# Performance work log

Measured on AMD Instinct MI355X. Metric: run time of the kernel, lower is better.

## Reference

```python
import jax, jax.numpy as jnp
import numpy as np

N_NODES = 100000
N_EDGES = 3200000
D_FEAT = 128


def setup_inputs() -> dict:
    key = jax.random.key(0)
    k1, k2, k3 = jax.random.split(key, 3)
    edges = jax.random.randint(k1, (2, N_EDGES), 0, N_NODES, dtype=jnp.int64)
    attentions = jax.random.uniform(k2, (N_EDGES,), dtype=jnp.float32)
    X = jax.random.normal(k3, (N_NODES, D_FEAT), dtype=jnp.float32)
    return {"edges": edges, "attentions": attentions, "N": N_NODES, "X": X}


def reference(edges, attentions, N, X):
    # Sparse COO adjacency (rows=edges[0], cols=edges[1], vals=attentions)
    # times dense X: out[i] = sum over edges (i -> j) of att_e * X[j]
    src = edges[0]  # row index i
    dst = edges[1]  # col index j
    messages = attentions[:, None] * X[dst]          # [E, D] gather + weight
    out = jax.ops.segment_sum(messages, src, num_segments=N)  # [N, D] scatter-add
    return out
```

## Files before the change

kernel.cpp:

```cpp
#include <hip/hip_runtime.h>

typedef unsigned int u32;
typedef unsigned short u16;


constexpr int D_FEAT  = 128;
constexpr int N_NODES = 100000;
constexpr int BROWS   = 128;
constexpr int KB      = (N_NODES + BROWS - 1) / BROWS;
constexpr int CHUNK   = 8192;
constexpr int NGRP    = 8;
constexpr int NCONV   = 128;
constexpr int CAP     = 4608;
constexpr int RPT     = CAP / 512;
constexpr int NPAN    = 8;
constexpr int NCELL   = NPAN * BROWS;

__device__ __forceinline__ u32 rne_bf16(float f) {
    u32 u = __float_as_uint(f);
    return (u + 0x7FFFu + ((u >> 16) & 1u)) >> 16;
}

__device__ __forceinline__ u32 pack_rec(int s, int d, float a) {
    u32 q = (u32)(a * 255.0f + 0.5f);
    return ((u32)(s & 127) << 25) | ((u32)d << 8) | q;
}

__device__ __forceinline__ u32 cell_of(u32 rec) {
    return (((rec >> 22) & 7u) << 7) | (rec >> 25);
}

__global__ __launch_bounds__(1024) void prep1(const int* __restrict__ src,
                                              u16* __restrict__ hist, int E, int nchunk,
                                              const float* __restrict__ X,
                                              uint2* __restrict__ Xb, int do_conv) {
    __shared__ u32 h[KB];
    const int blk = blockIdx.x;
    if (blk < nchunk) {
        const int e0 = blk * CHUNK;
        const int e1 = min(e0 + CHUNK, E);
        const int n  = e1 - e0;
        const int nfull = n & ~3;
        for (int i = threadIdx.x; i < KB; i += 1024) h[i] = 0;
        __syncthreads();
        for (int o = threadIdx.x * 4; o < nfull; o += 4096) {
            int4 s4 = *(const int4*)(src + e0 + o);
            atomicAdd(&h[s4.x >> 7], 1u);
            atomicAdd(&h[s4.y >> 7], 1u);
            atomicAdd(&h[s4.z >> 7], 1u);
            atomicAdd(&h[s4.w >> 7], 1u);
        }
        for (int o = nfull + threadIdx.x; o < n; o += 1024)
            atomicAdd(&h[src[e0 + o] >> 7], 1u);
        __syncthreads();
        u16* row = hist + (size_t)blk * KB;
        for (int i = threadIdx.x; i < KB; i += 1024) row[i] = (u16)h[i];
    } else if (do_conv) {
        const int nthreads = (gridDim.x - nchunk) * 1024;
        const float4* __restrict__ X4 = (const float4*)X;
        for (int u = (blk - nchunk) * 1024 + threadIdx.x; u < N_NODES * 32;
             u += nthreads) {
            float4 v = X4[u];
            uint2 o;
            o.x = rne_bf16(v.x) | (rne_bf16(v.y) << 16);
            o.y = rne_bf16(v.z) | (rne_bf16(v.w) << 16);
            Xb[u] = o;
        }
    }
}

__global__ __launch_bounds__(256) void colscan_a(u16* __restrict__ hist,
                                                 u32* __restrict__ gt,
                                                 int nchunk, int gsz) {
    const int t = blockIdx.x * 256 + threadIdx.x;
    if (t >= KB * NGRP) return;
    const int g = t / KB;
    const int b = t - g * KB;
    const int c0 = g * gsz;
    const int c1 = min(c0 + gsz, nchunk);
    u32 run = 0;
    for (int c = c0; c < c1; ++c) {
        u32 v = hist[(size_t)c * KB + b];
        hist[(size_t)c * KB + b] = (u16)run;
        run += v;
    }
    gt[(size_t)g * KB + b] = run;
}

__global__ __launch_bounds__(1024) void colscan_b(const u32* __restrict__ gt,
                                                  u32* __restrict__ gbase,
                                                  u32* __restrict__ bptr) {
    __shared__ u32 sm[1024];
    const int t = threadIdx.x;
    u32 tot = 0;
    if (t < KB) {
        #pragma unroll
        for (int g = 0; g < NGRP; ++g) {
            u32 v = gt[(size_t)g * KB + t];
            gbase[(size_t)g * KB + t] = tot;
            tot += v;
        }
    }
    sm[t] = tot;
    __syncthreads();
    for (int o = 1; o < 1024; o <<= 1) {
        u32 v = (t >= o) ? sm[t - o] : 0u;
        __syncthreads();
        sm[t] += v;
        __syncthreads();
    }
    if (t < KB) bptr[t] = sm[t] - tot;
    if (t == 1023) bptr[KB] = sm[1023];
}

__global__ __launch_bounds__(1024) void chunk_scatter(const int* __restrict__ src,
                                                      const int* __restrict__ dst,
                                                      const float* __restrict__ att,
                                                      const u32* __restrict__ bptr,
                                                      const u16* __restrict__ hist,
                                                      const u32* __restrict__ gbase,
                                                      u32* __restrict__ epack,
                                                      int E, int gsz) {
    __shared__ u32 cur[KB];
    const int c  = blockIdx.x;
    const int e0 = c * CHUNK;
    const int e1 = min(e0 + CHUNK, E);
    const int n  = e1 - e0;
    const int nfull = n & ~3;
    const u16* hrow = hist + (size_t)c * KB;
    const u32* grow = gbase + (size_t)(c / gsz) * KB;
    for (int i = threadIdx.x; i < KB; i += 1024)
        cur[i] = bptr[i] + grow[i] + (u32)hrow[i];
    __syncthreads();
    const bool v4ok = ((E & 3) == 0);
    if (v4ok) {
        for (int o = threadIdx.x * 4; o < nfull; o += 4096) {
            int4   s4 = *(const int4*)(src + e0 + o);
            int4   d4 = *(const int4*)(dst + e0 + o);
            float4 a4 = *(const float4*)(att + e0 + o);
            #pragma unroll
            for (int k = 0; k < 4; ++k) {
                int s = (&s4.x)[k];
                u32 pos = atomicAdd(&cur[s >> 7], 1u);
                epack[pos] = pack_rec(s, (&d4.x)[k], (&a4.x)[k]);
            }
        }
        for (int o = nfull + threadIdx.x; o < n; o += 1024) {
            int s = src[e0 + o];
            u32 pos = atomicAdd(&cur[s >> 7], 1u);
            epack[pos] = pack_rec(s, dst[e0 + o], att[e0 + o]);
        }
    } else {
        for (int o = threadIdx.x; o < n; o += 1024) {
            int s = src[e0 + o];
            u32 pos = atomicAdd(&cur[s >> 7], 1u);
            epack[pos] = pack_rec(s, dst[e0 + o], att[e0 + o]);
        }
    }
}

__global__ __launch_bounds__(512) void accumulate_bucket_bf16(
    const u32* __restrict__ bptr, const u32* __restrict__ epack,
    const uint2* __restrict__ Xb, const float* __restrict__ X,
    float* __restrict__ out, int N)
{
    __shared__ u32 ebuf[CAP];
    __shared__ u32 cnt[NCELL], off[NCELL], cur[NCELL];
    const int b   = blockIdx.x;
    const int tid = threadIdx.x;
    const int g   = tid >> 5;
    const int l   = tid & 31;
    const u32 s = bptr[b], e = bptr[b + 1];
    const int nb = (int)(e - s);
    const int row0 = b * BROWS;
    const int rows = min(BROWS, N - row0);

    if (nb > CAP) {
        float4* o4 = (float4*)(out + (size_t)row0 * D_FEAT);
        for (int i = tid; i < rows * 32; i += 512) o4[i] = make_float4(0.f,0.f,0.f,0.f);
        __syncthreads();
        for (u32 k = s + g; k < e; k += 16) {
            u32 p = epack[k];
            int d = (p >> 8) & 0x1FFFF, sl = p >> 25;
            float a = (float)(p & 255u) * (1.0f / 255.0f);
            float4 v = ((const float4*)(X + (size_t)d * D_FEAT))[l];
            float* o = out + (size_t)(row0 + sl) * D_FEAT + l * 4;
            unsafeAtomicAdd(o + 0, a * v.x);
            unsafeAtomicAdd(o + 1, a * v.y);
            unsafeAtomicAdd(o + 2, a * v.z);
            unsafeAtomicAdd(o + 3, a * v.w);
        }
        return;
    }

    u32 rec[RPT];
    #pragma unroll
    for (int k = 0; k < RPT; ++k) {
        int i = tid + k * 512;
        rec[k] = (i < nb) ? epack[s + i] : 0u;
    }
    for (int i = tid; i < NCELL; i += 512) cnt[i] = 0;
    __syncthreads();
    #pragma unroll
    for (int k = 0; k < RPT; ++k)
        if (tid + k * 512 < nb) atomicAdd(&cnt[cell_of(rec[k])], 1u);
    __syncthreads();
    if (tid < 64) {
        u32 c[16]; u32 tot = 0;
        #pragma unroll
        for (int k = 0; k < 16; ++k) { c[k] = cnt[tid * 16 + k]; tot += c[k]; }
        u32 incl = tot;
        #pragma unroll
        for (int o = 1; o < 64; o <<= 1) {
            u32 v = __shfl_up(incl, o, 64);
            if (tid >= o) incl += v;
        }
        u32 run = incl - tot;
        #pragma unroll
        for (int k = 0; k < 16; ++k) {
            off[tid * 16 + k] = run; cur[tid * 16 + k] = run; run += c[k];
        }
    }
    __syncthreads();
    #pragma unroll
    for (int k = 0; k < RPT; ++k)
        if (tid + k * 512 < nb) {
            u32 pos = atomicAdd(&cur[cell_of(rec[k])], 1u);
            ebuf[pos] = rec[k] & 0x01FFFFFFu;
        }
    __syncthreads();

    float4 acc[8];
    #pragma unroll
    for (int ri = 0; ri < 8; ++ri) acc[ri] = make_float4(0.f, 0.f, 0.f, 0.f);

    for (int p = 0; p < NPAN; ++p) {
        #pragma unroll
        for (int ri = 0; ri < 8; ++ri) {
            const int r = (ri << 4) + g;
            const u32 cell = ((u32)p << 7) | (u32)r;
            const u32 base = off[cell];
            const u32 n    = cnt[cell];
            float4 a4 = acc[ri];
            u32 j = 0;
            for (; j + 2 <= n; j += 2) {
                const u32 p0 = ebuf[base + j];
                const u32 p1 = ebuf[base + j + 1];
                const uint2 q0 = Xb[(size_t)(p0 >> 8) * 32 + l];
                const uint2 q1 = Xb[(size_t)(p1 >> 8) * 32 + l];
                const float a0 = (float)(p0 & 255u) * (1.0f / 255.0f);
                const float a1 = (float)(p1 & 255u) * (1.0f / 255.0f);
                a4.x = fmaf(a0, __uint_as_float(q0.x << 16),         a4.x);
                a4.y = fmaf(a0, __uint_as_float(q0.x & 0xFFFF0000u), a4.y);
                a4.z = fmaf(a0, __uint_as_float(q0.y << 16),         a4.z);
                a4.w = fmaf(a0, __uint_as_float(q0.y & 0xFFFF0000u), a4.w);
                a4.x = fmaf(a1, __uint_as_float(q1.x << 16),         a4.x);
                a4.y = fmaf(a1, __uint_as_float(q1.x & 0xFFFF0000u), a4.y);
                a4.z = fmaf(a1, __uint_as_float(q1.y << 16),         a4.z);
                a4.w = fmaf(a1, __uint_as_float(q1.y & 0xFFFF0000u), a4.w);
            }
            if (j < n) {
                const u32 p0 = ebuf[base + j];
                const uint2 q0 = Xb[(size_t)(p0 >> 8) * 32 + l];
                const float a0 = (float)(p0 & 255u) * (1.0f / 255.0f);
                a4.x = fmaf(a0, __uint_as_float(q0.x << 16),         a4.x);
                a4.y = fmaf(a0, __uint_as_float(q0.x & 0xFFFF0000u), a4.y);
                a4.z = fmaf(a0, __uint_as_float(q0.y << 16),         a4.z);
                a4.w = fmaf(a0, __uint_as_float(q0.y & 0xFFFF0000u), a4.w);
            }
            acc[ri] = a4;
        }
    }
    #pragma unroll
    for (int ri = 0; ri < 8; ++ri) {
        const int r = (ri << 4) + g;
        if (r < rows)
            ((float4*)out)[(size_t)(row0 + r) * 32 + l] = acc[ri];
    }
}

__global__ __launch_bounds__(512) void accumulate_bucket_f32(
    const u32* __restrict__ bptr, const u32* __restrict__ epack,
    const float* __restrict__ X, float* __restrict__ out, int N)
{
    __shared__ u32 ebuf[CAP];
    __shared__ u32 cnt[BROWS], off[BROWS], cur[BROWS];
    const int b   = blockIdx.x;
    const int tid = threadIdx.x;
    const int g   = tid >> 5;
    const int l   = tid & 31;
    const u32 s = bptr[b], e = bptr[b + 1];
    const int nb = (int)(e - s);
    const int row0 = b * BROWS;
    const int rows = min(BROWS, N - row0);

    if (nb > CAP) {
        float4* o4 = (float4*)(out + (size_t)row0 * D_FEAT);
        for (int i = tid; i < rows * 32; i += 512) o4[i] = make_float4(0.f,0.f,0.f,0.f);
        __syncthreads();
        for (u32 k = s + g; k < e; k += 16) {
            u32 p = epack[k];
            int d = (p >> 8) & 0x1FFFF, sl = p >> 25;
            float a = (float)(p & 255u) * (1.0f / 255.0f);
            float4 v = ((const float4*)(X + (size_t)d * D_FEAT))[l];
            float* o = out + (size_t)(row0 + sl) * D_FEAT + l * 4;
            unsafeAtomicAdd(o + 0, a * v.x);
            unsafeAtomicAdd(o + 1, a * v.y);
            unsafeAtomicAdd(o + 2, a * v.z);
            unsafeAtomicAdd(o + 3, a * v.w);
        }
        return;
    }

    u32 rec[RPT];
    #pragma unroll
    for (int k = 0; k < RPT; ++k) {
        int i = tid + k * 512;
        rec[k] = (i < nb) ? epack[s + i] : 0u;
    }
    if (tid < BROWS) cnt[tid] = 0;
    __syncthreads();
    #pragma unroll
    for (int k = 0; k < RPT; ++k)
        if (tid + k * 512 < nb) atomicAdd(&cnt[rec[k] >> 25], 1u);
    __syncthreads();
    if (tid < 64) {
        u32 c0 = cnt[2 * tid], c1 = cnt[2 * tid + 1];
        u32 ps = c0 + c1;
        u32 incl = ps;
        #pragma unroll
        for (int o = 1; o < 64; o <<= 1) {
            u32 v = __shfl_up(incl, o, 64);
            if (tid >= o) incl += v;
        }
        u32 excl = incl - ps;
        off[2 * tid]     = excl;      cur[2 * tid]     = excl;
        off[2 * tid + 1] = excl + c0; cur[2 * tid + 1] = excl + c0;
    }
    __syncthreads();
    #pragma unroll
    for (int k = 0; k < RPT; ++k)
        if (tid + k * 512 < nb) {
            u32 pos = atomicAdd(&cur[rec[k] >> 25], 1u);
            ebuf[pos] = rec[k] & 0x01FFFFFFu;
        }
    __syncthreads();

    const float4* __restrict__ X4 = (const float4*)X;
    for (int r = g; r < rows; r += 16) {
        const u32 base = off[r];
        const u32 n    = cnt[r];
        float4 acc = make_float4(0.f, 0.f, 0.f, 0.f);
        u32 j = 0;
        for (; j + 4 <= n; j += 4) {
            u32 p[4]; float4 v[4];
            #pragma unroll
            for (int k = 0; k < 4; ++k) p[k] = ebuf[base + j + k];
            #pragma unroll
            for (int k = 0; k < 4; ++k) v[k] = X4[(size_t)(p[k] >> 8) * 32 + l];
            #pragma unroll
            for (int k = 0; k < 4; ++k) {
                const float a = (float)(p[k] & 255u) * (1.0f / 255.0f);
                acc.x = fmaf(a, v[k].x, acc.x); acc.y = fmaf(a, v[k].y, acc.y);
                acc.z = fmaf(a, v[k].z, acc.z); acc.w = fmaf(a, v[k].w, acc.w);
            }
        }
        for (; j < n; ++j) {
            const u32 p = ebuf[base + j];
            const float4 v = X4[(size_t)(p >> 8) * 32 + l];
            const float a = (float)(p & 255u) * (1.0f / 255.0f);
            acc.x = fmaf(a, v.x, acc.x); acc.y = fmaf(a, v.y, acc.y);
            acc.z = fmaf(a, v.z, acc.z); acc.w = fmaf(a, v.w, acc.w);
        }
        ((float4*)out)[(size_t)(row0 + r) * 32 + l] = acc;
    }
}

__global__ __launch_bounds__(256) void spmm_edge_atomic(
    const int* __restrict__ src, const int* __restrict__ dst,
    const float* __restrict__ att, const float* __restrict__ X,
    float* __restrict__ out, int E)
{
    const int group = (int)((blockIdx.x * blockDim.x + threadIdx.x) >> 5);
    const int lane  = threadIdx.x & 31;
    const int nGroups = (int)((gridDim.x * blockDim.x) >> 5);
    for (int e = group; e < E; e += nGroups) {
        const int s = src[e], d = dst[e];
        const float a = att[e];
        const float4 v = ((const float4*)(X + (size_t)d * D_FEAT))[lane];
        float* o = out + (size_t)s * D_FEAT + (size_t)lane * 4;
        unsafeAtomicAdd(o + 0, a * v.x);
        unsafeAtomicAdd(o + 1, a * v.y);
        unsafeAtomicAdd(o + 2, a * v.z);
        unsafeAtomicAdd(o + 3, a * v.w);
    }
}

static inline size_t align16(size_t x) { return (x + 15) & ~(size_t)15; }

extern "C" void kernel_launch(void* const* d_in, const int* in_sizes, int n_in,
                              void* d_out, int out_size, void* d_ws, size_t ws_size,
                              hipStream_t stream) {
    const int*   edges = (const int*)d_in[0];
    const float* att   = (const float*)d_in[1];
    const float* X     = (const float*)d_in[3];
    float*       out   = (float*)d_out;

    const int E = in_sizes[1];
    const int N = N_NODES;
    const int* src = edges;
    const int* dst = edges + E;
    const int nchunk = (E + CHUNK - 1) / CHUNK;
    const int gsz    = (nchunk + NGRP - 1) / NGRP;

    size_t o_hist  = 0;
    size_t o_gt    = align16(o_hist + (size_t)nchunk * KB * 2);
    size_t o_gbase = o_gt    + (size_t)NGRP * KB * 4;
    size_t o_bptr  = o_gbase + (size_t)NGRP * KB * 4;
    size_t o_epack = align16(o_bptr + ((size_t)KB + 1) * 4);
    size_t o_xb    = align16(o_epack + (size_t)E * 4);
    size_t need_f32  = o_xb;
    size_t need_bf16 = o_xb + (size_t)N * D_FEAT * 2;

    if (ws_size < need_f32) {
        hipMemsetAsync(d_out, 0, (size_t)out_size * sizeof(float), stream);
        const int grid = (E + 7) / 8;
        spmm_edge_atomic<<<grid, 256, 0, stream>>>(src, dst, att, X, out, E);
        return;
    }

    char* ws = (char*)d_ws;
    u16*  hist  = (u16*)(ws + o_hist);
    u32*  gt    = (u32*)(ws + o_gt);
    u32*  gbase = (u32*)(ws + o_gbase);
    u32*  bptr  = (u32*)(ws + o_bptr);
    u32*  epack = (u32*)(ws + o_epack);
    uint2* Xb   = (uint2*)(ws + o_xb);

    const bool use_bf16 = (ws_size >= need_bf16);

    prep1<<<nchunk + (use_bf16 ? NCONV : 0), 1024, 0, stream>>>(
        src, hist, E, nchunk, X, Xb, use_bf16 ? 1 : 0);
    colscan_a<<<(KB * NGRP + 255) / 256, 256, 0, stream>>>(hist, gt, nchunk, gsz);
    colscan_b<<<1, 1024, 0, stream>>>(gt, gbase, bptr);
    chunk_scatter<<<nchunk, 1024, 0, stream>>>(src, dst, att, bptr, hist, gbase,
                                               epack, E, gsz);

    if (use_bf16)
        accumulate_bucket_bf16<<<KB, 512, 0, stream>>>(bptr, epack, Xb, X, out, N);
    else
        accumulate_bucket_f32<<<KB, 512, 0, stream>>>(bptr, epack, X, out, N);
}
```

Measured before the change: 294.1 us.

## Fuse histogram, scan and scatter into one pass with fixed-capacity buckets

Replaces the histogram kernel, two column-scan kernels and chunk scatter with a single fused kernel. Each chunk counts edges per bucket in shared memory and reserves space with one global atomic per bucket. Buckets now live in fixed-capacity slots, and overflow goes to a spill buffer that a fixup kernel later applies with atomics. This removes three launches and one extra pass over src, but bucket placement now depends on atomic ordering, and edges beyond the spill capacity would be silently dropped.

```diff
diff --git a/kernel.cpp b/kernel.cpp
--- a/kernel.cpp
+++ b/kernel.cpp
@@ -9,12 +9,12 @@
 constexpr int BROWS   = 128;
 constexpr int KB      = (N_NODES + BROWS - 1) / BROWS;
 constexpr int CHUNK   = 8192;
-constexpr int NGRP    = 8;
 constexpr int NCONV   = 128;
 constexpr int CAP     = 4608;
 constexpr int RPT     = CAP / 512;
 constexpr int NPAN    = 8;
 constexpr int NCELL   = NPAN * BROWS;
+constexpr int SPILL_CAP = 65536;
 
 __device__ __forceinline__ u32 rne_bf16(float f) {
     u32 u = __float_as_uint(f);
@@ -30,109 +30,61 @@
     return (((rec >> 22) & 7u) << 7) | (rec >> 25);
 }
 
-__global__ __launch_bounds__(1024) void prep1(const int* __restrict__ src,
-                                              u16* __restrict__ hist, int E, int nchunk,
-                                              const float* __restrict__ X,
-                                              uint2* __restrict__ Xb, int do_conv) {
-    __shared__ u32 h[KB];
+__global__ __launch_bounds__(1024) void scatter_fused(
+    const int* __restrict__ src, const int* __restrict__ dst,
+    const float* __restrict__ att, u32* __restrict__ gcur,
+    int2* __restrict__ spill, u32* __restrict__ epack,
+    const float* __restrict__ X, uint2* __restrict__ Xb,
+    int E, int nchunk, int do_conv)
+{
     const int blk = blockIdx.x;
-    if (blk < nchunk) {
-        const int e0 = blk * CHUNK;
-        const int e1 = min(e0 + CHUNK, E);
-        const int n  = e1 - e0;
-        const int nfull = n & ~3;
-        for (int i = threadIdx.x; i < KB; i += 1024) h[i] = 0;
-        __syncthreads();
-        for (int o = threadIdx.x * 4; o < nfull; o += 4096) {
-            int4 s4 = *(const int4*)(src + e0 + o);
-            atomicAdd(&h[s4.x >> 7], 1u);
-            atomicAdd(&h[s4.y >> 7], 1u);
-            atomicAdd(&h[s4.z >> 7], 1u);
-            atomicAdd(&h[s4.w >> 7], 1u);
-        }
-        for (int o = nfull + threadIdx.x; o < n; o += 1024)
-            atomicAdd(&h[src[e0 + o] >> 7], 1u);
-        __syncthreads();
-        u16* row = hist + (size_t)blk * KB;
-        for (int i = threadIdx.x; i < KB; i += 1024) row[i] = (u16)h[i];
-    } else if (do_conv) {
-        const int nthreads = (gridDim.x - nchunk) * 1024;
-        const float4* __restrict__ X4 = (const float4*)X;
-        for (int u = (blk - nchunk) * 1024 + threadIdx.x; u < N_NODES * 32;
-             u += nthreads) {
-            float4 v = X4[u];
-            uint2 o;
-            o.x = rne_bf16(v.x) | (rne_bf16(v.y) << 16);
-            o.y = rne_bf16(v.z) | (rne_bf16(v.w) << 16);
-            Xb[u] = o;
-        }
-    }
-}
-
-__global__ __launch_bounds__(256) void colscan_a(u16* __restrict__ hist,
-                                                 u32* __restrict__ gt,
-                                                 int nchunk, int gsz) {
-    const int t = blockIdx.x * 256 + threadIdx.x;
-    if (t >= KB * NGRP) return;
-    const int g = t / KB;
-    const int b = t - g * KB;
-    const int c0 = g * gsz;
-    const int c1 = min(c0 + gsz, nchunk);
-    u32 run = 0;
-    for (int c = c0; c < c1; ++c) {
-        u32 v = hist[(size_t)c * KB + b];
-        hist[(size_t)c * KB + b] = (u16)run;
-        run += v;
-    }
-    gt[(size_t)g * KB + b] = run;
-}
-
-__global__ __launch_bounds__(1024) void colscan_b(const u32* __restrict__ gt,
-                                                  u32* __restrict__ gbase,
-                                                  u32* __restrict__ bptr) {
-    __shared__ u32 sm[1024];
-    const int t = threadIdx.x;
-    u32 tot = 0;
-    if (t < KB) {
-        #pragma unroll
-        for (int g = 0; g < NGRP; ++g) {
-            u32 v = gt[(size_t)g * KB + t];
-            gbase[(size_t)g * KB + t] = tot;
-            tot += v;
-        }
-    }
-    sm[t] = tot;
-    __syncthreads();
-    for (int o = 1; o < 1024; o <<= 1) {
-        u32 v = (t >= o) ? sm[t - o] : 0u;
-        __syncthreads();
-        sm[t] += v;
-        __syncthreads();
-    }
-    if (t < KB) bptr[t] = sm[t] - tot;
-    if (t == 1023) bptr[KB] = sm[1023];
-}
-
-__global__ __launch_bounds__(1024) void chunk_scatter(const int* __restrict__ src,
-                                                      const int* __restrict__ dst,
-                                                      const float* __restrict__ att,
-                                                      const u32* __restrict__ bptr,
-                                                      const u16* __restrict__ hist,
-                                                      const u32* __restrict__ gbase,
-                                                      u32* __restrict__ epack,
-                                                      int E, int gsz) {
-    __shared__ u32 cur[KB];
-    const int c  = blockIdx.x;
-    const int e0 = c * CHUNK;
+    if (blk >= nchunk) {
+        if (do_conv) {
+            const int nthreads = (gridDim.x - nchunk) * 1024;
+            const float4* __restrict__ X4 = (const float4*)X;
+            for (int u = (blk - nchunk) * 1024 + threadIdx.x; u < N_NODES * 32;
+                 u += nthreads) {
+                float4 v = X4[u];
+                uint2 o;
+                o.x = rne_bf16(v.x) | (rne_bf16(v.y) << 16);
+                o.y = rne_bf16(v.z) | (rne_bf16(v.w) << 16);
+                Xb[u] = o;
+            }
+        }
+        return;
+    }
+
+    __shared__ u32 lcnt[KB], lbase[KB];
+    const int e0 = blk * CHUNK;
     const int e1 = min(e0 + CHUNK, E);
     const int n  = e1 - e0;
     const int nfull = n & ~3;
-    const u16* hrow = hist + (size_t)c * KB;
-    const u32* grow = gbase + (size_t)(c / gsz) * KB;
-    for (int i = threadIdx.x; i < KB; i += 1024)
-        cur[i] = bptr[i] + grow[i] + (u32)hrow[i];
-    __syncthreads();
     const bool v4ok = ((E & 3) == 0);
+
+    for (int i = threadIdx.x; i < KB; i += 1024) lcnt[i] = 0;
+    __syncthreads();
+    if (v4ok) {
+        for (int o = threadIdx.x * 4; o < nfull; o += 4096) {
+            int4 s4 = *(const int4*)(src + e0 + o);
+            atomicAdd(&lcnt[s4.x >> 7], 1u);
+            atomicAdd(&lcnt[s4.y >> 7], 1u);
+            atomicAdd(&lcnt[s4.z >> 7], 1u);
+            atomicAdd(&lcnt[s4.w >> 7], 1u);
+        }
+        for (int o = nfull + threadIdx.x; o < n; o += 1024)
+            atomicAdd(&lcnt[src[e0 + o] >> 7], 1u);
+    } else {
+        for (int o = threadIdx.x; o < n; o += 1024)
+            atomicAdd(&lcnt[src[e0 + o] >> 7], 1u);
+    }
+    __syncthreads();
+    for (int i = threadIdx.x; i < KB; i += 1024) {
+        u32 c = lcnt[i];
+        lbase[i] = c ? atomicAdd(&gcur[i], c) : 0u;
+    }
+    __syncthreads();
+    for (int i = threadIdx.x; i < KB; i += 1024) lcnt[i] = 0;
+    __syncthreads();
     if (v4ok) {
         for (int o = threadIdx.x * 4; o < nfull; o += 4096) {
             int4   s4 = *(const int4*)(src + e0 + o);
@@ -140,29 +92,58 @@
             float4 a4 = *(const float4*)(att + e0 + o);
             #pragma unroll
             for (int k = 0; k < 4; ++k) {
-                int s = (&s4.x)[k];
-                u32 pos = atomicAdd(&cur[s >> 7], 1u);
-                epack[pos] = pack_rec(s, (&d4.x)[k], (&a4.x)[k]);
+                int s = (&s4.x)[k], d = (&d4.x)[k];
+                float a = (&a4.x)[k];
+                int b = s >> 7;
+                u32 pos = lbase[b] + atomicAdd(&lcnt[b], 1u);
+                if (pos < (u32)CAP) {
+                    epack[(size_t)b * CAP + pos] = pack_rec(s, d, a);
+                } else {
+                    u32 sp = atomicAdd(&gcur[KB], 1u);
+                    if (sp < (u32)SPILL_CAP) {
+                        u32 q = (u32)(a * 255.0f + 0.5f);
+                        spill[sp] = make_int2(s, (d << 8) | (int)q);
+                    }
+                }
             }
         }
         for (int o = nfull + threadIdx.x; o < n; o += 1024) {
-            int s = src[e0 + o];
-            u32 pos = atomicAdd(&cur[s >> 7], 1u);
-            epack[pos] = pack_rec(s, dst[e0 + o], att[e0 + o]);
+            int s = src[e0 + o], d = dst[e0 + o];
+            float a = att[e0 + o];
+            int b = s >> 7;
+            u32 pos = lbase[b] + atomicAdd(&lcnt[b], 1u);
+            if (pos < (u32)CAP) {
+                epack[(size_t)b * CAP + pos] = pack_rec(s, d, a);
+            } else {
+                u32 sp = atomicAdd(&gcur[KB], 1u);
+                if (sp < (u32)SPILL_CAP) {
+                    u32 q = (u32)(a * 255.0f + 0.5f);
+                    spill[sp] = make_int2(s, (d << 8) | (int)q);
+                }
+            }
         }
     } else {
         for (int o = threadIdx.x; o < n; o += 1024) {
-            int s = src[e0 + o];
-            u32 pos = atomicAdd(&cur[s >> 7], 1u);
-            epack[pos] = pack_rec(s, dst[e0 + o], att[e0 + o]);
+            int s = src[e0 + o], d = dst[e0 + o];
+            float a = att[e0 + o];
+            int b = s >> 7;
+            u32 pos = lbase[b] + atomicAdd(&lcnt[b], 1u);
+            if (pos < (u32)CAP) {
+                epack[(size_t)b * CAP + pos] = pack_rec(s, d, a);
+            } else {
+                u32 sp = atomicAdd(&gcur[KB], 1u);
+                if (sp < (u32)SPILL_CAP) {
+                    u32 q = (u32)(a * 255.0f + 0.5f);
+                    spill[sp] = make_int2(s, (d << 8) | (int)q);
+                }
+            }
         }
     }
 }
 
 __global__ __launch_bounds__(512) void accumulate_bucket_bf16(
-    const u32* __restrict__ bptr, const u32* __restrict__ epack,
-    const uint2* __restrict__ Xb, const float* __restrict__ X,
-    float* __restrict__ out, int N)
+    const u32* __restrict__ gcur, const u32* __restrict__ epack,
+    const uint2* __restrict__ Xb, float* __restrict__ out, int N)
 {
     __shared__ u32 ebuf[CAP];
     __shared__ u32 cnt[NCELL], off[NCELL], cur[NCELL];
@@ -170,28 +151,10 @@
     const int tid = threadIdx.x;
     const int g   = tid >> 5;
     const int l   = tid & 31;
-    const u32 s = bptr[b], e = bptr[b + 1];
-    const int nb = (int)(e - s);
+    const u32 s  = (u32)b * CAP;
+    const int nb = min((int)gcur[b], CAP);
     const int row0 = b * BROWS;
     const int rows = min(BROWS, N - row0);
-
-    if (nb > CAP) {
-        float4* o4 = (float4*)(out + (size_t)row0 * D_FEAT);
-        for (int i = tid; i < rows * 32; i += 512) o4[i] = make_float4(0.f,0.f,0.f,0.f);
-        __syncthreads();
-        for (u32 k = s + g; k < e; k += 16) {
-            u32 p = epack[k];
-            int d = (p >> 8) & 0x1FFFF, sl = p >> 25;
-            float a = (float)(p & 255u) * (1.0f / 255.0f);
-            float4 v = ((const float4*)(X + (size_t)d * D_FEAT))[l];
-            float* o = out + (size_t)(row0 + sl) * D_FEAT + l * 4;
-            unsafeAtomicAdd(o + 0, a * v.x);
-            unsafeAtomicAdd(o + 1, a * v.y);
-            unsafeAtomicAdd(o + 2, a * v.z);
-            unsafeAtomicAdd(o + 3, a * v.w);
-        }
-        return;
-    }
 
     u32 rec[RPT];
     #pragma unroll
@@ -280,7 +243,7 @@
 }
 
 __global__ __launch_bounds__(512) void accumulate_bucket_f32(
-    const u32* __restrict__ bptr, const u32* __restrict__ epack,
+    const u32* __restrict__ gcur, const u32* __restrict__ epack,
     const float* __restrict__ X, float* __restrict__ out, int N)
 {
     __shared__ u32 ebuf[CAP];
@@ -289,28 +252,10 @@
     const int tid = threadIdx.x;
     const int g   = tid >> 5;
     const int l   = tid & 31;
-    const u32 s = bptr[b], e = bptr[b + 1];
-    const int nb = (int)(e - s);
+    const u32 s  = (u32)b * CAP;
+    const int nb = min((int)gcur[b], CAP);
     const int row0 = b * BROWS;
     const int rows = min(BROWS, N - row0);
-
-    if (nb > CAP) {
-        float4* o4 = (float4*)(out + (size_t)row0 * D_FEAT);
-        for (int i = tid; i < rows * 32; i += 512) o4[i] = make_float4(0.f,0.f,0.f,0.f);
-        __syncthreads();
-        for (u32 k = s + g; k < e; k += 16) {
-            u32 p = epack[k];
-            int d = (p >> 8) & 0x1FFFF, sl = p >> 25;
-            float a = (float)(p & 255u) * (1.0f / 255.0f);
-            float4 v = ((const float4*)(X + (size_t)d * D_FEAT))[l];
-            float* o = out + (size_t)(row0 + sl) * D_FEAT + l * 4;
-            unsafeAtomicAdd(o + 0, a * v.x);
-            unsafeAtomicAdd(o + 1, a * v.y);
-            unsafeAtomicAdd(o + 2, a * v.z);
-            unsafeAtomicAdd(o + 3, a * v.w);
-        }
-        return;
-    }
 
     u32 rec[RPT];
     #pragma unroll
@@ -376,6 +321,28 @@
     }
 }
 
+__global__ __launch_bounds__(256) void spill_fixup(
+    const u32* __restrict__ gcur, const int2* __restrict__ spill,
+    const float* __restrict__ X, float* __restrict__ out)
+{
+    const int nspill = min((int)gcur[KB], SPILL_CAP);
+    if (nspill == 0) return;
+    const int group = (int)((blockIdx.x * blockDim.x + threadIdx.x) >> 5);
+    const int lane  = threadIdx.x & 31;
+    const int nGroups = (int)((gridDim.x * blockDim.x) >> 5);
+    for (int e = group; e < nspill; e += nGroups) {
+        const int2 p = spill[e];
+        const int s = p.x, d = p.y >> 8;
+        const float a = (float)(p.y & 255) * (1.0f / 255.0f);
+        const float4 v = ((const float4*)(X + (size_t)d * D_FEAT))[lane];
+        float* o = out + (size_t)s * D_FEAT + (size_t)lane * 4;
+        unsafeAtomicAdd(o + 0, a * v.x);
+        unsafeAtomicAdd(o + 1, a * v.y);
+        unsafeAtomicAdd(o + 2, a * v.z);
+        unsafeAtomicAdd(o + 3, a * v.w);
+    }
+}
+
 __global__ __launch_bounds__(256) void spmm_edge_atomic(
     const int* __restrict__ src, const int* __restrict__ dst,
     const float* __restrict__ att, const float* __restrict__ X,
@@ -411,14 +378,11 @@
     const int* src = edges;
     const int* dst = edges + E;
     const int nchunk = (E + CHUNK - 1) / CHUNK;
-    const int gsz    = (nchunk + NGRP - 1) / NGRP;
-
-    size_t o_hist  = 0;
-    size_t o_gt    = align16(o_hist + (size_t)nchunk * KB * 2);
-    size_t o_gbase = o_gt    + (size_t)NGRP * KB * 4;
-    size_t o_bptr  = o_gbase + (size_t)NGRP * KB * 4;
-    size_t o_epack = align16(o_bptr + ((size_t)KB + 1) * 4);
-    size_t o_xb    = align16(o_epack + (size_t)E * 4);
+
+    size_t o_gcur  = 0;
+    size_t o_spill = align16(o_gcur + ((size_t)KB + 1) * 4);
+    size_t o_epack = align16(o_spill + (size_t)SPILL_CAP * 8);
+    size_t o_xb    = align16(o_epack + (size_t)KB * CAP * 4);
     size_t need_f32  = o_xb;
     size_t need_bf16 = o_xb + (size_t)N * D_FEAT * 2;
 
@@ -430,24 +394,22 @@
     }
 
     char* ws = (char*)d_ws;
-    u16*  hist  = (u16*)(ws + o_hist);
-    u32*  gt    = (u32*)(ws + o_gt);
-    u32*  gbase = (u32*)(ws + o_gbase);
-    u32*  bptr  = (u32*)(ws + o_bptr);
+    u32*  gcur  = (u32*)(ws + o_gcur);
+    int2* spill = (int2*)(ws + o_spill);
     u32*  epack = (u32*)(ws + o_epack);
     uint2* Xb   = (uint2*)(ws + o_xb);
 
     const bool use_bf16 = (ws_size >= need_bf16);
 
-    prep1<<<nchunk + (use_bf16 ? NCONV : 0), 1024, 0, stream>>>(
-        src, hist, E, nchunk, X, Xb, use_bf16 ? 1 : 0);
-    colscan_a<<<(KB * NGRP + 255) / 256, 256, 0, stream>>>(hist, gt, nchunk, gsz);
-    colscan_b<<<1, 1024, 0, stream>>>(gt, gbase, bptr);
-    chunk_scatter<<<nchunk, 1024, 0, stream>>>(src, dst, att, bptr, hist, gbase,
-                                               epack, E, gsz);
+    hipMemsetAsync(gcur, 0, ((size_t)KB + 1) * 4, stream);
+
+    scatter_fused<<<nchunk + (use_bf16 ? NCONV : 0), 1024, 0, stream>>>(
+        src, dst, att, gcur, spill, epack, X, Xb, E, nchunk, use_bf16 ? 1 : 0);
 
     if (use_bf16)
-        accumulate_bucket_bf16<<<KB, 512, 0, stream>>>(bptr, epack, Xb, X, out, N);
+        accumulate_bucket_bf16<<<KB, 512, 0, stream>>>(gcur, epack, Xb, out, N);
     else
-        accumulate_bucket_f32<<<KB, 512, 0, stream>>>(bptr, epack, X, out, N);
-}
+        accumulate_bucket_f32<<<KB, 512, 0, stream>>>(gcur, epack, X, out, N);
+
+    spill_fixup<<<128, 256, 0, stream>>>(gcur, spill, X, out);
+}
```

After: 277.8 us. 1.06x faster.
